# Kernel tuning notes

Measured on AMD Instinct MI355X. Metric: run time of the kernel, lower is better.

The kernel has to match this reference:

```python
import jax, jax.numpy as jnp
import numpy as np

# Static configuration (values of input_spatial_shapes are compile-time constants,
# mirroring how Deformable DETR fixes the FPN level sizes per image resolution).
SPATIAL_SHAPES = [(128, 128), (64, 64), (32, 32), (16, 16)]
N_HEADS = 8
N_LEVELS = 4
N_POINTS = 4
D_MODEL = 256
HEAD_DIM = D_MODEL // N_HEADS  # 32


def setup_inputs() -> dict:
    key = jax.random.key(0)
    ks = jax.random.split(key, 12)
    n = 1
    len_in = sum(h * w for h, w in SPATIAL_SHAPES)  # 21760
    len_q = len_in
    s = 0.02
    inp = {
        "query": jax.random.normal(ks[0], (n, len_q, D_MODEL), jnp.float32),
        "reference_points": jax.random.uniform(ks[1], (n, len_q, N_LEVELS, 2), jnp.float32),
        "input_flatten": jax.random.normal(ks[2], (n, len_in, D_MODEL), jnp.float32),
        "input_spatial_shapes": jnp.array(SPATIAL_SHAPES, jnp.int32),
        "input_level_start_index": jnp.array(
            np.cumsum([0] + [h * w for h, w in SPATIAL_SHAPES[:-1]]), jnp.int32
        ),
        # learned parameters (nn.Linear stores weight as [out, in])
        "W_off": jax.random.normal(ks[3], (N_HEADS * N_LEVELS * N_POINTS * 2, D_MODEL), jnp.float32) * s,
        "b_off": jax.random.normal(ks[4], (N_HEADS * N_LEVELS * N_POINTS * 2,), jnp.float32) * 0.5,
        "W_attn": jax.random.normal(ks[5], (N_HEADS * N_LEVELS * N_POINTS, D_MODEL), jnp.float32) * s,
        "b_attn": jnp.zeros((N_HEADS * N_LEVELS * N_POINTS,), jnp.float32),
        "W_val": jax.random.normal(ks[6], (D_MODEL, D_MODEL), jnp.float32) * s,
        "b_val": jnp.zeros((D_MODEL,), jnp.float32),
        "W_out": jax.random.normal(ks[7], (D_MODEL, D_MODEL), jnp.float32) * s,
        "b_out": jnp.zeros((D_MODEL,), jnp.float32),
    }
    return inp


def _bilinear_sample(img, grid, h, w):
    """torch F.grid_sample(mode='bilinear', padding_mode='zeros', align_corners=False).
    img:  [B, C, h, w]; grid: [B, Q, P, 2] in [-1, 1] -> returns [B, C, Q, P]."""
    B, C = img.shape[0], img.shape[1]
    Q, P = grid.shape[1], grid.shape[2]
    gx = (grid[..., 0] + 1.0) * (w * 0.5) - 0.5
    gy = (grid[..., 1] + 1.0) * (h * 0.5) - 0.5
    x0 = jnp.floor(gx)
    y0 = jnp.floor(gy)
    lx, ly = gx - x0, gy - y0
    x0i = x0.astype(jnp.int32)
    y0i = y0.astype(jnp.int32)
    flat = img.reshape(B, C, h * w)
    acc = jnp.zeros((B, C, Q * P), img.dtype)
    for dx, dy, wgt in (
        (0, 0, (1 - lx) * (1 - ly)),
        (1, 0, lx * (1 - ly)),
        (0, 1, (1 - lx) * ly),
        (1, 1, lx * ly),
    ):
        xi = x0i + dx
        yi = y0i + dy
        valid = (xi >= 0) & (xi < w) & (yi >= 0) & (yi < h)
        idx = (jnp.clip(yi, 0, h - 1) * w + jnp.clip(xi, 0, w - 1)).reshape(B, Q * P)
        vals = jnp.take_along_axis(flat, jnp.broadcast_to(idx[:, None, :], (B, C, Q * P)), axis=2)
        acc = acc + vals * (wgt * valid.astype(img.dtype)).reshape(B, 1, Q * P)
    return acc.reshape(B, C, Q, P)


def reference(query, reference_points, input_flatten, input_spatial_shapes,
              input_level_start_index, W_off, b_off, W_attn, b_attn,
              W_val, b_val, W_out, b_out):
    n, Q, C = query.shape
    # value projection
    value = input_flatten @ W_val.T + b_val                      # [n, Lin, C]
    value = value.reshape(n, -1, N_HEADS, HEAD_DIM)              # [n, Lin, H, D]
    # sampling offsets & attention weights from query
    off = (query @ W_off.T + b_off).reshape(n, Q, N_HEADS, N_LEVELS, N_POINTS, 2)
    aw = jax.nn.softmax(
        (query @ W_attn.T + b_attn).reshape(n, Q, N_HEADS, N_LEVELS * N_POINTS), axis=-1
    ).reshape(n, Q, N_HEADS, N_LEVELS, N_POINTS)
    # reference_points has last dim 2: normalize offsets by (w, h) per level
    norm = jnp.array([[w, h] for h, w in SPATIAL_SHAPES], jnp.float32)  # [L, 2]
    loc = reference_points[:, :, None, :, None, :] + off / norm[None, None, None, :, None, :]
    grids = 2.0 * loc - 1.0                                       # [n,Q,H,L,P,2]
    aw_t = aw.transpose(0, 2, 1, 3, 4).reshape(n * N_HEADS, 1, Q, N_LEVELS, N_POINTS)
    out = jnp.zeros((n * N_HEADS, HEAD_DIM, Q), query.dtype)
    start = 0
    for lvl, (h, w) in enumerate(SPATIAL_SHAPES):
        v = value[:, start:start + h * w]                         # [n, hw, H, D]
        start += h * w
        img = v.transpose(0, 2, 3, 1).reshape(n * N_HEADS, HEAD_DIM, h, w)
        g = grids[:, :, :, lvl].transpose(0, 2, 1, 3, 4).reshape(n * N_HEADS, Q, N_POINTS, 2)
        sampled = _bilinear_sample(img, g, h, w)                  # [nH, D, Q, P]
        out = out + (sampled * aw_t[:, :, :, lvl, :]).sum(-1)
    out = out.reshape(n, N_HEADS * HEAD_DIM, Q).transpose(0, 2, 1)  # [n, Q, C]
    return out @ W_out.T + b_out
```

## Files before the change

### kernel.cpp

```cpp
#include <hip/hip_runtime.h>
#include <math.h>

#define Q_TOTAL 21760
#define QB 16
#define HEAD_IMG_BYTES 1392640

typedef _Float16     f16;
typedef short        s16x8 __attribute__((ext_vector_type(8)));
typedef f16          f16x8 __attribute__((ext_vector_type(8)));
typedef f16          f16x4 __attribute__((ext_vector_type(4)));
typedef f16          f16x2 __attribute__((ext_vector_type(2)));
typedef __bf16       bfv8  __attribute__((ext_vector_type(8)));
typedef float        f32x4 __attribute__((ext_vector_type(4)));
typedef float        f32x2 __attribute__((ext_vector_type(2)));
typedef unsigned int u32x4 __attribute__((ext_vector_type(4)));
typedef unsigned int u32x2 __attribute__((ext_vector_type(2)));

__device__ __forceinline__ s16x8 pack8(float4 a, float4 b) {
    bfv8 t;
    t[0] = (__bf16)a.x; t[1] = (__bf16)a.y; t[2] = (__bf16)a.z; t[3] = (__bf16)a.w;
    t[4] = (__bf16)b.x; t[5] = (__bf16)b.y; t[6] = (__bf16)b.z; t[7] = (__bf16)b.w;
    return __builtin_bit_cast(s16x8, t);
}

__global__ __launch_bounds__(256) void cvt_weights(
    const float* __restrict__ Woff, const float* __restrict__ Wattn,
    const float* __restrict__ Wval, const float* __restrict__ Wout,
    const float* __restrict__ boff, const float* __restrict__ battn,
    unsigned short* __restrict__ dst, float* __restrict__ bias_cat)
{
    if (blockIdx.x == 224) {
        const int t = threadIdx.x;
        bias_cat[t] = boff[t];
        if (t < 128) bias_cat[256 + t] = battn[t];
        return;
    }
    const int e = blockIdx.x * 1024 + threadIdx.x * 4;
    const float* src; int base;
    if (e < 65536)       { src = Woff;  base = 0; }
    else if (e < 98304)  { src = Wattn; base = 65536; }
    else if (e < 163840) { src = Wval;  base = 98304; }
    else                 { src = Wout;  base = 163840; }
    float4 v = *(const float4*)(src + (e - base));
    ushort4 o;
    o.x = __builtin_bit_cast(unsigned short, (__bf16)v.x);
    o.y = __builtin_bit_cast(unsigned short, (__bf16)v.y);
    o.z = __builtin_bit_cast(unsigned short, (__bf16)v.z);
    o.w = __builtin_bit_cast(unsigned short, (__bf16)v.w);
    *(ushort4*)(dst + e) = o;
}

__global__ __launch_bounds__(256) void gemm_proj(
    const float* __restrict__ input_flatten,
    const float* __restrict__ query,
    const unsigned short* __restrict__ w16,
    const float* __restrict__ b_val,
    const float* __restrict__ bias_cat,
    f16* __restrict__ value_t,
    f16* __restrict__ offattn)
{
    constexpr int K = 256, BM = 64, BN = 128;
    constexpr int NB2 = BN / 2;
    constexpr int NF = NB2 / 16;
    __shared__ unsigned short As[BM * 32];
    __shared__ unsigned short Bs[BN * 32];

    const int tid  = threadIdx.x;
    const int lane = tid & 63;
    const int wv   = tid >> 6;
    const int wr   = wv >> 1, wc = wv & 1;
    const int rowBase = blockIdx.x * BM;
    const int slab = blockIdx.y;

    const float* A32 = (slab < 2) ? input_flatten : query;
    int wbase;
    switch (slab) {
        case 0:  wbase = 98304;  break;
        case 1:  wbase = 131072; break;
        case 2:  wbase = 0;      break;
        case 3:  wbase = 32768;  break;
        default: wbase = 65536;  break;
    }
    const unsigned short* Wp0 = w16 + wbase;
    const float* bias = (slab < 2) ? (b_val + slab * 128) : (bias_cat + (slab - 2) * 128);

    const int sr    = tid >> 2;
    const int skq   = (tid & 3) * 8;
    const int sslot = (tid & 3) * 16;

    f32x4 acc[2][NF];
#pragma unroll
    for (int i = 0; i < 2; i++)
#pragma unroll
        for (int j = 0; j < NF; j++) acc[i][j] = (f32x4){0.f, 0.f, 0.f, 0.f};

    const float* Ap = A32 + (size_t)(rowBase + sr) * K + skq;

    for (int kt = 0; kt < K; kt += 32) {
        s16x8 aval = pack8(*(const float4*)(Ap + kt), *(const float4*)(Ap + kt + 4));
        s16x8 bval[2];
#pragma unroll
        for (int c = 0; c < 2; c++) {
            const unsigned short* p = Wp0 + (size_t)(c * 64 + sr) * K + kt + skq;
            bval[c] = *(const s16x8*)p;
        }
        __syncthreads();
        *(s16x8*)(As + (((sr * 64 + sslot) ^ ((sr & 7) << 4)) >> 1)) = aval;
#pragma unroll
        for (int c = 0; c < 2; c++) {
            const int row = c * 64 + sr;
            *(s16x8*)(Bs + (((row * 64 + sslot) ^ ((row & 7) << 4)) >> 1)) = bval[c];
        }
        __syncthreads();
        s16x8 af[2];
#pragma unroll
        for (int mi = 0; mi < 2; mi++) {
            const int row = wr * 32 + mi * 16 + (lane & 15);
            af[mi] = *(const s16x8*)(As + (((row * 64 + (lane >> 4) * 16) ^ ((row & 7) << 4)) >> 1));
        }
#pragma unroll
        for (int ni = 0; ni < NF; ni++) {
            const int row = wc * NB2 + ni * 16 + (lane & 15);
            s16x8 bfrag = *(const s16x8*)(Bs + (((row * 64 + (lane >> 4) * 16) ^ ((row & 7) << 4)) >> 1));
#pragma unroll
            for (int mi = 0; mi < 2; mi++)
                acc[mi][ni] = __builtin_amdgcn_mfma_f32_16x16x32_bf16(af[mi], bfrag, acc[mi][ni], 0, 0, 0);
        }
    }

#pragma unroll
    for (int ni = 0; ni < NF; ni++) {
        const int localcol = wc * NB2 + ni * 16 + (lane & 15);
        const float bv = bias[localcol];
#pragma unroll
        for (int mi = 0; mi < 2; mi++) {
            const int r0 = rowBase + wr * 32 + mi * 16 + (lane >> 4) * 4;
#pragma unroll
            for (int j = 0; j < 4; j++) {
                const float v = acc[mi][ni][j] + bv;
                const int row = r0 + j;
                if (slab < 2) {
                    const int col = slab * 128 + localcol;
                    value_t[((size_t)(col >> 5) * Q_TOTAL + row) * 32 + (col & 31)] = (f16)v;
                } else {
                    const int col = (slab - 2) * 128 + localcol;
                    offattn[(size_t)row * 384 + col] = (f16)v;
                }
            }
        }
    }
}

__global__ __launch_bounds__(256) void gemm_out(
    const unsigned short* __restrict__ A16,
    const unsigned short* __restrict__ W16,
    const float* __restrict__ bias,
    float* __restrict__ C)
{
    constexpr int K = 256, BM = 64, BN = 128;
    constexpr int NB2 = BN / 2;
    constexpr int NF = NB2 / 16;
    __shared__ unsigned short As[BM * 32];
    __shared__ unsigned short Bs[BN * 32];

    const int tid  = threadIdx.x;
    const int lane = tid & 63;
    const int wv   = tid >> 6;
    const int wr   = wv >> 1, wc = wv & 1;
    const int rowBase = blockIdx.x * BM;
    const int colBase = blockIdx.y * BN;

    const int sr    = tid >> 2;
    const int skq   = (tid & 3) * 8;
    const int sslot = (tid & 3) * 16;

    f32x4 acc[2][NF];
#pragma unroll
    for (int i = 0; i < 2; i++)
#pragma unroll
        for (int j = 0; j < NF; j++) acc[i][j] = (f32x4){0.f, 0.f, 0.f, 0.f};

    const unsigned short* Ap = A16 + (size_t)(rowBase + sr) * K + skq;

    for (int kt = 0; kt < K; kt += 32) {
        s16x8 aval = *(const s16x8*)(Ap + kt);
        s16x8 bval[2];
#pragma unroll
        for (int c = 0; c < 2; c++) {
            const unsigned short* p = W16 + (size_t)(colBase + c * 64 + sr) * K + kt + skq;
            bval[c] = *(const s16x8*)p;
        }
        __syncthreads();
        *(s16x8*)(As + (((sr * 64 + sslot) ^ ((sr & 7) << 4)) >> 1)) = aval;
#pragma unroll
        for (int c = 0; c < 2; c++) {
            const int row = c * 64 + sr;
            *(s16x8*)(Bs + (((row * 64 + sslot) ^ ((row & 7) << 4)) >> 1)) = bval[c];
        }
        __syncthreads();
        s16x8 af[2];
#pragma unroll
        for (int mi = 0; mi < 2; mi++) {
            const int row = wr * 32 + mi * 16 + (lane & 15);
            af[mi] = *(const s16x8*)(As + (((row * 64 + (lane >> 4) * 16) ^ ((row & 7) << 4)) >> 1));
        }
#pragma unroll
        for (int ni = 0; ni < NF; ni++) {
            const int row = wc * NB2 + ni * 16 + (lane & 15);
            s16x8 bfrag = *(const s16x8*)(Bs + (((row * 64 + (lane >> 4) * 16) ^ ((row & 7) << 4)) >> 1));
#pragma unroll
            for (int mi = 0; mi < 2; mi++)
                acc[mi][ni] = __builtin_amdgcn_mfma_f32_16x16x32_bf16(af[mi], bfrag, acc[mi][ni], 0, 0, 0);
        }
    }

#pragma unroll
    for (int ni = 0; ni < NF; ni++) {
        const int col = colBase + wc * NB2 + ni * 16 + (lane & 15);
        const float bv = bias[col];
#pragma unroll
        for (int mi = 0; mi < 2; mi++) {
            const int r0 = rowBase + wr * 32 + mi * 16 + (lane >> 4) * 4;
#pragma unroll
            for (int j = 0; j < 4; j++)
                C[(size_t)(r0 + j) * 256 + col] = acc[mi][ni][j] + bv;
        }
    }
}

__global__ __launch_bounds__(256) void sample_kernel(
    const f16* __restrict__ value_t,
    const f16* __restrict__ offattn,
    const float* __restrict__ refpts,
    unsigned short* __restrict__ sampled)
{
    __shared__ __attribute__((aligned(16))) unsigned s_iw[32 * 132];

    const int tid   = threadIdx.x;
    const int qt    = blockIdx.x >> 2;
    const int hp    = blockIdx.x & 3;
    const int qbase = qt * QB;

    {
        const int q  = tid >> 4;
        const int h  = (tid >> 3) & 1;
        const int l  = (tid >> 1) & 3;
        const int ph = tid & 1;
        const int H  = hp * 2 + h;
        const int g  = tid >> 3;
        const f16* oa = offattn + (size_t)(qbase + q) * 384;

        f16x2 lgh = *(const f16x2*)(oa + 256 + H * 16 + l * 4 + ph * 2);
        const float lg0 = (float)lgh[0], lg1 = (float)lgh[1];
        float m = fmaxf(lg0, lg1);
        m = fmaxf(m, __shfl_xor(m, 1));
        m = fmaxf(m, __shfl_xor(m, 2));
        m = fmaxf(m, __shfl_xor(m, 4));
        float e0 = __expf(lg0 - m), e1 = __expf(lg1 - m);
        float s = e0 + e1;
        s += __shfl_xor(s, 1);
        s += __shfl_xor(s, 2);
        s += __shfl_xor(s, 4);
        const float inv = 1.f / s;
        const float aw2[2] = {e0 * inv, e1 * inv};

        f16x4 offh = *(const f16x4*)(oa + H * 32 + l * 8 + ph * 4);
        f32x2 rp = *(const f32x2*)(refpts + (size_t)(qbase + q) * 8 + l * 2);

        const int   SZ[4] = {128, 64, 32, 16};
        const int   ST[4] = {0, 16384, 20480, 21504};
        const int   W_ = SZ[l], START = ST[l];
        const float S = (float)W_;

        unsigned* dst = &s_iw[g * 132 + (l * 4 + ph * 2) * 8];
#pragma unroll
        for (int c = 0; c < 2; c++) {
            const float ox = (float)offh[c * 2], oy = (float)offh[c * 2 + 1];
            const float a = aw2[c];
            const float gx = fmaf(rp[0], S, ox) - 0.5f;
            const float gy = fmaf(rp[1], S, oy) - 0.5f;
            const float x0f = floorf(gx), y0f = floorf(gy);
            const float lx = gx - x0f, ly = gy - y0f;
            const int x0 = (int)x0f, y0 = (int)y0f;
            const int xs  = min(max(x0, 0), W_ - 2);
            const int sft = xs - x0;
            const float wx0 = (x0 >= 0 && x0 < W_) ? (1.f - lx) : 0.f;
            const float wx1 = (x0 + 1 >= 0 && x0 + 1 < W_) ? lx : 0.f;
            const float wxA = (sft == 0) ? wx0 : ((sft == 1) ? wx1 : 0.f);
            const float wxB = (sft == 0) ? wx1 : ((sft == -1) ? wx0 : 0.f);
            const int y1 = y0 + 1;
            const int y0c = min(max(y0, 0), W_ - 1);
            const int y1c = min(max(y1, 0), W_ - 1);
            const float wy0a = (((y0 >= 0) && (y0 < W_)) ? (1.f - ly) : 0.f) * a;
            const float wy1a = (((y1 >= 0) && (y1 < W_)) ? ly : 0.f) * a;
            const unsigned o0 = (unsigned)((START + y0c * W_ + xs) * 64);
            const unsigned o1 = (unsigned)((START + y1c * W_ + xs) * 64);
            u32x4 r0, r1;
            r0[0] = o0;      r0[1] = o1;
            r0[2] = __float_as_uint(wy0a * wxA);
            r0[3] = __float_as_uint(wy1a * wxA);
            r1[0] = o0 + 64; r1[1] = o1 + 64;
            r1[2] = __float_as_uint(wy0a * wxB);
            r1[3] = __float_as_uint(wy1a * wxB);
            *(u32x4*)(dst + c * 8)     = r0;
            *(u32x4*)(dst + c * 8 + 4) = r1;
        }
    }
    __syncthreads();

    {
        const int d8 = tid & 3;
        const int xc = (tid >> 2) & 1;
        const int g  = tid >> 3;
        const int q  = g >> 1;
        const int h  = g & 1;
        const int H  = hp * 2 + h;
        const unsigned vbase = (unsigned)(H * HEAD_IMG_BYTES) + (unsigned)(d8 * 16);
        const char* vt = (const char*)value_t;
        const unsigned* iw = &s_iw[g * 132 + xc * 4];

        float acc[8] = {0.f, 0.f, 0.f, 0.f, 0.f, 0.f, 0.f, 0.f};
#pragma unroll
        for (int half = 0; half < 2; half++) {
            u32x2 off[8];
#pragma unroll
            for (int p = 0; p < 8; p++)
                off[p] = *(const u32x2*)(iw + (half * 8 + p) * 8);
            f16x8 v0[8], v1[8];
#pragma unroll
            for (int p = 0; p < 8; p++) {
                v0[p] = *(const f16x8*)(vt + (size_t)(vbase + off[p][0]));
                v1[p] = *(const f16x8*)(vt + (size_t)(vbase + off[p][1]));
            }
#pragma unroll
            for (int p = 0; p < 8; p++) {
                const f32x2 w = *(const f32x2*)(iw + (half * 8 + p) * 8 + 2);
#pragma unroll
                for (int r = 0; r < 8; r++) {
                    acc[r] = fmaf((float)v0[p][r], w[0], acc[r]);
                    acc[r] = fmaf((float)v1[p][r], w[1], acc[r]);
                }
            }
        }
#pragma unroll
        for (int j = 0; j < 8; j++) acc[j] += __shfl_xor(acc[j], 4);

        if (xc == 0) {
            s16x8 o = pack8(make_float4(acc[0], acc[1], acc[2], acc[3]),
                            make_float4(acc[4], acc[5], acc[6], acc[7]));
            *(s16x8*)(sampled + (size_t)(qbase + q) * 256 + H * 32 + d8 * 8) = o;
        }
    }
}

extern "C" void kernel_launch(void* const* d_in, const int* in_sizes, int n_in,
                              void* d_out, int out_size, void* d_ws, size_t ws_size,
                              hipStream_t stream) {
    const float* query  = (const float*)d_in[0];
    const float* refpts = (const float*)d_in[1];
    const float* input_flatten = (const float*)d_in[2];
    const float* W_off  = (const float*)d_in[5];
    const float* b_off  = (const float*)d_in[6];
    const float* W_attn = (const float*)d_in[7];
    const float* b_attn = (const float*)d_in[8];
    const float* W_val  = (const float*)d_in[9];
    const float* b_val  = (const float*)d_in[10];
    const float* W_out  = (const float*)d_in[11];
    const float* b_out  = (const float*)d_in[12];
    float* out = (float*)d_out;

    char* ws = (char*)d_ws;
    f16*            value_t = (f16*)ws;
    f16*            offattn = (f16*)(ws + 11141120);
    unsigned short* sampled = (unsigned short*)(ws + 27852800);
    unsigned short* w16     = (unsigned short*)(ws + 38993920);
    float*          bias_cat= (float*)(ws + 39452672);

    cvt_weights<<<225, 256, 0, stream>>>(W_off, W_attn, W_val, W_out, b_off, b_attn, w16, bias_cat);

    gemm_proj<<<dim3(340, 5), 256, 0, stream>>>(input_flatten, query, w16,
                                                b_val, bias_cat, value_t, offattn);
    sample_kernel<<<dim3((Q_TOTAL / QB) * 4), 256, 0, stream>>>(value_t, offattn, refpts, sampled);
    gemm_out<<<dim3(340, 2), 256, 0, stream>>>(sampled, w16 + 163840, b_out, out);
}
```

Baseline: 80.16 us.

## Pre-tile and pre-swizzle bf16 weights, stage B tiles via global_load_lds

The weight conversion kernel now writes bf16 weights in per-k-tile, pre-swizzled 8KB blocks matching the LDS layout. Both GEMM kernels can then copy B tiles straight into shared memory with global_load_lds instead of loading through registers and storing. The bias concatenation is dropped and biases are read directly. This cuts register traffic and VGPR pressure in the GEMM loops, but relies on the async LDS load completing before the barrier and on the tile layout being exactly right.

```diff
diff --git a/kernel.cpp b/kernel.cpp
--- a/kernel.cpp
+++ b/kernel.cpp
@@ -23,39 +23,44 @@
     return __builtin_bit_cast(s16x8, t);
 }
 
-__global__ __launch_bounds__(256) void cvt_weights(
+__device__ __forceinline__ void gload_lds16(const void* g, void* l) {
+    auto gp = (const __attribute__((address_space(1))) unsigned int*)(g);
+    auto lp = (__attribute__((address_space(3))) unsigned int*)(l);
+    __builtin_amdgcn_global_load_lds(gp, lp, 16, 0, 0);
+}
+
+__global__ __launch_bounds__(256) void cvt_tiles(
     const float* __restrict__ Woff, const float* __restrict__ Wattn,
     const float* __restrict__ Wval, const float* __restrict__ Wout,
-    const float* __restrict__ boff, const float* __restrict__ battn,
-    unsigned short* __restrict__ dst, float* __restrict__ bias_cat)
+    unsigned short* __restrict__ w16t)
 {
-    if (blockIdx.x == 224) {
-        const int t = threadIdx.x;
-        bias_cat[t] = boff[t];
-        if (t < 128) bias_cat[256 + t] = battn[t];
-        return;
-    }
-    const int e = blockIdx.x * 1024 + threadIdx.x * 4;
-    const float* src; int base;
-    if (e < 65536)       { src = Woff;  base = 0; }
-    else if (e < 98304)  { src = Wattn; base = 65536; }
-    else if (e < 163840) { src = Wval;  base = 98304; }
-    else                 { src = Wout;  base = 163840; }
-    float4 v = *(const float4*)(src + (e - base));
-    ushort4 o;
-    o.x = __builtin_bit_cast(unsigned short, (__bf16)v.x);
-    o.y = __builtin_bit_cast(unsigned short, (__bf16)v.y);
-    o.z = __builtin_bit_cast(unsigned short, (__bf16)v.z);
-    o.w = __builtin_bit_cast(unsigned short, (__bf16)v.w);
-    *(ushort4*)(dst + e) = o;
+    const int c = blockIdx.x * 256 + threadIdx.x;
+    const int t = c >> 9;
+    const int q = (c & 511) * 16;
+    const int r = q >> 6;
+    const int i = q & 63;
+    const int dstb = t * 8192 + (q ^ ((r & 7) << 4));
+    const int kelem = (t & 7) * 32 + (i >> 1);
+    const float* src; int rowbase;
+    if (t < 8)       { src = Wval;  rowbase = 0;   }
+    else if (t < 16) { src = Wval;  rowbase = 128; }
+    else if (t < 24) { src = Woff;  rowbase = 0;   }
+    else if (t < 32) { src = Woff;  rowbase = 128; }
+    else if (t < 40) { src = Wattn; rowbase = 0;   }
+    else if (t < 48) { src = Wout;  rowbase = 0;   }
+    else             { src = Wout;  rowbase = 128; }
+    const float* p = src + (size_t)(rowbase + r) * 256 + kelem;
+    s16x8 v = pack8(*(const float4*)p, *(const float4*)(p + 4));
+    *(s16x8*)((char*)w16t + dstb) = v;
 }
 
 __global__ __launch_bounds__(256) void gemm_proj(
     const float* __restrict__ input_flatten,
     const float* __restrict__ query,
-    const unsigned short* __restrict__ w16,
+    const unsigned short* __restrict__ w16t,
     const float* __restrict__ b_val,
-    const float* __restrict__ bias_cat,
+    const float* __restrict__ b_off,
+    const float* __restrict__ b_attn,
     f16* __restrict__ value_t,
     f16* __restrict__ offattn)
 {
@@ -73,20 +78,19 @@
     const int slab = blockIdx.y;
 
     const float* A32 = (slab < 2) ? input_flatten : query;
-    int wbase;
-    switch (slab) {
-        case 0:  wbase = 98304;  break;
-        case 1:  wbase = 131072; break;
-        case 2:  wbase = 0;      break;
-        case 3:  wbase = 32768;  break;
-        default: wbase = 65536;  break;
-    }
-    const unsigned short* Wp0 = w16 + wbase;
-    const float* bias = (slab < 2) ? (b_val + slab * 128) : (bias_cat + (slab - 2) * 128);
+    const float* bias;
+    if (slab < 2)       bias = b_val + slab * 128;
+    else if (slab == 2) bias = b_off;
+    else if (slab == 3) bias = b_off + 128;
+    else                bias = b_attn;
+
+    const char* Btiles = (const char*)w16t + (size_t)slab * 65536;
 
     const int sr    = tid >> 2;
     const int skq   = (tid & 3) * 8;
     const int sslot = (tid & 3) * 16;
+    const int wbase = wv * 1024;
+    const int t16   = tid * 16;
 
     f32x4 acc[2][NF];
 #pragma unroll
@@ -96,32 +100,25 @@
 
     const float* Ap = A32 + (size_t)(rowBase + sr) * K + skq;
 
-    for (int kt = 0; kt < K; kt += 32) {
+    for (int kti = 0; kti < 8; kti++) {
+        const int kt = kti * 32;
         s16x8 aval = pack8(*(const float4*)(Ap + kt), *(const float4*)(Ap + kt + 4));
-        s16x8 bval[2];
-#pragma unroll
-        for (int c = 0; c < 2; c++) {
-            const unsigned short* p = Wp0 + (size_t)(c * 64 + sr) * K + kt + skq;
-            bval[c] = *(const s16x8*)p;
-        }
         __syncthreads();
-        *(s16x8*)(As + (((sr * 64 + sslot) ^ ((sr & 7) << 4)) >> 1)) = aval;
-#pragma unroll
-        for (int c = 0; c < 2; c++) {
-            const int row = c * 64 + sr;
-            *(s16x8*)(Bs + (((row * 64 + sslot) ^ ((row & 7) << 4)) >> 1)) = bval[c];
-        }
+        const char* bsrc = Btiles + kti * 8192;
+        gload_lds16(bsrc + t16,        (char*)Bs + wbase);
+        gload_lds16(bsrc + 4096 + t16, (char*)Bs + 4096 + wbase);
+        *(s16x8*)((char*)As + ((sr * 64 + sslot) ^ ((sr & 7) << 4))) = aval;
         __syncthreads();
         s16x8 af[2];
 #pragma unroll
         for (int mi = 0; mi < 2; mi++) {
             const int row = wr * 32 + mi * 16 + (lane & 15);
-            af[mi] = *(const s16x8*)(As + (((row * 64 + (lane >> 4) * 16) ^ ((row & 7) << 4)) >> 1));
+            af[mi] = *(const s16x8*)((char*)As + ((row * 64 + (lane >> 4) * 16) ^ ((row & 7) << 4)));
         }
 #pragma unroll
         for (int ni = 0; ni < NF; ni++) {
             const int row = wc * NB2 + ni * 16 + (lane & 15);
-            s16x8 bfrag = *(const s16x8*)(Bs + (((row * 64 + (lane >> 4) * 16) ^ ((row & 7) << 4)) >> 1));
+            s16x8 bfrag = *(const s16x8*)((char*)Bs + ((row * 64 + (lane >> 4) * 16) ^ ((row & 7) << 4)));
 #pragma unroll
             for (int mi = 0; mi < 2; mi++)
                 acc[mi][ni] = __builtin_amdgcn_mfma_f32_16x16x32_bf16(af[mi], bfrag, acc[mi][ni], 0, 0, 0);
@@ -153,7 +150,7 @@
 
 __global__ __launch_bounds__(256) void gemm_out(
     const unsigned short* __restrict__ A16,
-    const unsigned short* __restrict__ W16,
+    const unsigned short* __restrict__ w16t,
     const float* __restrict__ bias,
     float* __restrict__ C)
 {
@@ -170,9 +167,13 @@
     const int rowBase = blockIdx.x * BM;
     const int colBase = blockIdx.y * BN;
 
+    const char* Btiles = (const char*)w16t + 327680 + (size_t)blockIdx.y * 65536;
+
     const int sr    = tid >> 2;
     const int skq   = (tid & 3) * 8;
     const int sslot = (tid & 3) * 16;
+    const int wbase = wv * 1024;
+    const int t16   = tid * 16;
 
     f32x4 acc[2][NF];
 #pragma unroll
@@ -182,32 +183,25 @@
 
     const unsigned short* Ap = A16 + (size_t)(rowBase + sr) * K + skq;
 
-    for (int kt = 0; kt < K; kt += 32) {
+    for (int kti = 0; kti < 8; kti++) {
+        const int kt = kti * 32;
         s16x8 aval = *(const s16x8*)(Ap + kt);
-        s16x8 bval[2];
-#pragma unroll
-        for (int c = 0; c < 2; c++) {
-            const unsigned short* p = W16 + (size_t)(colBase + c * 64 + sr) * K + kt + skq;
-            bval[c] = *(const s16x8*)p;
-        }
         __syncthreads();
-        *(s16x8*)(As + (((sr * 64 + sslot) ^ ((sr & 7) << 4)) >> 1)) = aval;
-#pragma unroll
-        for (int c = 0; c < 2; c++) {
-            const int row = c * 64 + sr;
-            *(s16x8*)(Bs + (((row * 64 + sslot) ^ ((row & 7) << 4)) >> 1)) = bval[c];
-        }
+        const char* bsrc = Btiles + kti * 8192;
+        gload_lds16(bsrc + t16,        (char*)Bs + wbase);
+        gload_lds16(bsrc + 4096 + t16, (char*)Bs + 4096 + wbase);
+        *(s16x8*)((char*)As + ((sr * 64 + sslot) ^ ((sr & 7) << 4))) = aval;
         __syncthreads();
         s16x8 af[2];
 #pragma unroll
         for (int mi = 0; mi < 2; mi++) {
             const int row = wr * 32 + mi * 16 + (lane & 15);
-            af[mi] = *(const s16x8*)(As + (((row * 64 + (lane >> 4) * 16) ^ ((row & 7) << 4)) >> 1));
+            af[mi] = *(const s16x8*)((char*)As + ((row * 64 + (lane >> 4) * 16) ^ ((row & 7) << 4)));
         }
 #pragma unroll
         for (int ni = 0; ni < NF; ni++) {
             const int row = wc * NB2 + ni * 16 + (lane & 15);
-            s16x8 bfrag = *(const s16x8*)(Bs + (((row * 64 + (lane >> 4) * 16) ^ ((row & 7) << 4)) >> 1));
+            s16x8 bfrag = *(const s16x8*)((char*)Bs + ((row * 64 + (lane >> 4) * 16) ^ ((row & 7) << 4)));
 #pragma unroll
             for (int mi = 0; mi < 2; mi++)
                 acc[mi][ni] = __builtin_amdgcn_mfma_f32_16x16x32_bf16(af[mi], bfrag, acc[mi][ni], 0, 0, 0);
@@ -373,13 +367,12 @@
     f16*            value_t = (f16*)ws;
     f16*            offattn = (f16*)(ws + 11141120);
     unsigned short* sampled = (unsigned short*)(ws + 27852800);
-    unsigned short* w16     = (unsigned short*)(ws + 38993920);
-    float*          bias_cat= (float*)(ws + 39452672);
-
-    cvt_weights<<<225, 256, 0, stream>>>(W_off, W_attn, W_val, W_out, b_off, b_attn, w16, bias_cat);
-
-    gemm_proj<<<dim3(340, 5), 256, 0, stream>>>(input_flatten, query, w16,
-                                                b_val, bias_cat, value_t, offattn);
+    unsigned short* w16t    = (unsigned short*)(ws + 38993920);
+
+    cvt_tiles<<<112, 256, 0, stream>>>(W_off, W_attn, W_val, W_out, w16t);
+
+    gemm_proj<<<dim3(340, 5), 256, 0, stream>>>(input_flatten, query, w16t,
+                                                b_val, b_off, b_attn, value_t, offattn);
     sample_kernel<<<dim3((Q_TOTAL / QB) * 4), 256, 0, stream>>>(value_t, offattn, refpts, sampled);
-    gemm_out<<<dim3(340, 2), 256, 0, stream>>>(sampled, w16 + 163840, b_out, out);
-}
+    gemm_out<<<dim3(340, 2), 256, 0, stream>>>(sampled, w16t, b_out, out);
+}
```

Result: no change. 80.05 us (median of 2 runs) (-0.1%).
